# Performance work log

Measured on AMD Instinct MI355X. Metric: run time of the kernel, lower is better.

## Reference

```python
import jax, jax.numpy as jnp
import numpy as np

H, KVH, HD = 32, 8, 128
DM = 4096
LN_L, LN_R = 64, 64
K_BITS, V_BITS = 4, 4
ROPE_THETA = 10000.0


def _rope(x, pos):
    # x: [B, nH, S, D], pos: [B, S]
    D = x.shape[-1]
    inv_freq = 1.0 / (ROPE_THETA ** (jnp.arange(0, D, 2, dtype=jnp.float32) / D))
    freqs = pos[:, :, None].astype(jnp.float32) * inv_freq            # [B,S,D/2]
    emb = jnp.concatenate([freqs, freqs], axis=-1)                     # [B,S,D]
    cos = jnp.cos(emb)[:, None, :, :]
    sin = jnp.sin(emb)[:, None, :, :]
    x1, x2 = x[..., : D // 2], x[..., D // 2:]
    rot = jnp.concatenate([-x2, x1], axis=-1)
    return x * cos + rot * sin


def _fake_quant(x, bits):
    # per-token (last-dim row) symmetric fake quantization
    qmax = 2.0 ** (bits - 1) - 1.0
    s = jnp.maximum(jnp.max(jnp.abs(x), axis=-1, keepdims=True) / qmax, 1e-8)
    return jnp.clip(jnp.round(x / s), -qmax, qmax) * s


def setup_inputs() -> dict:
    key = jax.random.key(0)
    ks = jax.random.split(key, 10)
    B, S = 1, 2048
    hidden_states = jax.random.normal(ks[0], (B, S, DM), dtype=jnp.float32)
    causal = jnp.tril(jnp.ones((S, S), dtype=bool))
    attention_mask = jnp.where(causal, 0.0, -1e9).astype(jnp.float32)[None, None]  # [1,1,S,S]
    position_ids = jnp.arange(S, dtype=jnp.int32)[None, :]
    sc = 1.0 / np.sqrt(DM)
    Wq = jax.random.normal(ks[1], (DM, H * HD), dtype=jnp.float32) * sc
    Wk = jax.random.normal(ks[2], (DM, KVH * HD), dtype=jnp.float32) * sc
    Wv = jax.random.normal(ks[3], (DM, KVH * HD), dtype=jnp.float32) * sc
    Wo = jax.random.normal(ks[4], (H * HD, DM), dtype=jnp.float32) * (1.0 / np.sqrt(H * HD))
    ln_left = jnp.eye(LN_L, dtype=jnp.float32) + 0.02 * jax.random.normal(ks[5], (LN_L, LN_L), dtype=jnp.float32)
    ln_right = jnp.eye(LN_R, dtype=jnp.float32) + 0.02 * jax.random.normal(ks[6], (LN_R, LN_R), dtype=jnp.float32)
    Tk = jnp.eye(HD, dtype=jnp.float32) + 0.05 * jax.random.normal(ks[7], (HD, HD), dtype=jnp.float32)
    Tv = jnp.eye(HD, dtype=jnp.float32) + 0.05 * jax.random.normal(ks[8], (HD, HD), dtype=jnp.float32)
    return {"hidden_states": hidden_states, "attention_mask": attention_mask,
            "position_ids": position_ids, "ln_left": ln_left, "ln_right": ln_right,
            "Wq": Wq, "Wk": Wk, "Wv": Wv, "Wo": Wo, "Tk": Tk, "Tv": Tv}


def reference(hidden_states, attention_mask, position_ids,
              ln_left, ln_right, Wq, Wk, Wv, Wo, Tk, Tv):
    B, S, _ = hidden_states.shape
    # ln_trans: Kronecker-decomposed SVD transform on hidden dim (64x64)
    h = hidden_states.reshape(B, S, LN_L, LN_R)
    h = jnp.einsum('bslr,la,rc->bsac', h, ln_left, ln_right).reshape(B, S, DM)
    # q/k/v projections (effective, trans-absorbed weights)
    q = (h @ Wq).reshape(B, S, H, HD).transpose(0, 2, 1, 3)    # [B,H,S,hd]
    k = (h @ Wk).reshape(B, S, KVH, HD).transpose(0, 2, 1, 3)  # [B,KVH,S,hd]
    v = ((h @ Wv).reshape(B, S, KVH, HD) @ Tv).transpose(0, 2, 1, 3)  # vcache_trans on V
    # RoPE
    q = _rope(q, position_ids)
    k = _rope(k, position_ids)
    # kcache_trans: q gets inv-transpose, k gets forward transform, then fake-quant K
    Tk_inv_t = jnp.linalg.inv(Tk).T
    q = q @ Tk_inv_t
    k = _fake_quant(k @ Tk, K_BITS)
    # vcache quant
    v = _fake_quant(v, V_BITS)
    # GQA repeat
    rep = H // KVH
    k = jnp.repeat(k, rep, axis=1)
    v = jnp.repeat(v, rep, axis=1)
    scores = jnp.einsum('bhqd,bhkd->bhqk', q, k) / np.sqrt(HD) + attention_mask
    p = jax.nn.softmax(scores.astype(jnp.float32), axis=-1).astype(q.dtype)
    o = jnp.einsum('bhqk,bhkd->bhqd', p, v).transpose(0, 2, 1, 3)  # [B,S,H,hd]
    # undo vcache_trans per head, then output projection
    o = o @ jnp.linalg.inv(Tv)
    return o.reshape(B, S, DM) @ Wo
```

## Files before the change

kernel.cpp:

```cpp
#include <hip/hip_runtime.h>
#include <math.h>

#define S_    2048
#define DM_   4096
#define H_    32
#define KVH_  8
#define HD_   128

typedef __bf16 bf16x8 __attribute__((ext_vector_type(8)));
typedef float  f32x4  __attribute__((ext_vector_type(4)));
typedef unsigned short u16x8 __attribute__((ext_vector_type(8)));
typedef unsigned short ushort_t;

__device__ __forceinline__ ushort_t f2b(float f) {
  unsigned int u = __float_as_uint(f);
  unsigned int r = (u + 0x7fffu + ((u >> 16) & 1u)) >> 16;
  return (ushort_t)r;
}
__device__ __forceinline__ float b2f(ushort_t h) {
  return __uint_as_float(((unsigned int)h) << 16);
}
__device__ __forceinline__ bf16x8 asbf(u16x8 v) {
  return __builtin_bit_cast(bf16x8, v);
}

__device__ __forceinline__ void gload16(const void* g, void* l) {
  __builtin_amdgcn_global_load_lds(
      (const __attribute__((address_space(1))) void*)g,
      (__attribute__((address_space(3))) void*)(unsigned int)(unsigned long long)l,
      16, 0, 0);
}

__global__ void newton_init(const float* __restrict__ A0, const float* __restrict__ A1,
                            float* __restrict__ X0, float* __restrict__ X1)
{
  const float* A = blockIdx.x ? A1 : A0;
  float*       X = blockIdx.x ? X1 : X0;
  const int i = blockIdx.y * 1024 + threadIdx.x;
  const int r = i >> 7, c = i & 127;
  X[i] = ((r == c) ? 2.0f : 0.0f) - A[i];
}

__global__ __launch_bounds__(256) void nmm(
    const float* __restrict__ A0, const float* __restrict__ B0, float* __restrict__ C0, int tr0,
    const float* __restrict__ A1, const float* __restrict__ B1, float* __restrict__ C1, int tr1,
    int update)
{
  const float* A = blockIdx.y ? A1 : A0;
  const float* B = blockIdx.y ? B1 : B0;
  float*       C = blockIdx.y ? C1 : C0;
  const int tr   = blockIdx.y ? tr1 : tr0;
  const int m0   = blockIdx.x * 32;
  const int tid  = threadIdx.x;

  __shared__ float Bs[128][132];
  __shared__ float As[32][132];

#pragma unroll
  for (int i = 0; i < 16; ++i) {
    int idx = tid + i * 256;
    int row = idx >> 5, c4 = (idx & 31) * 4;
    *(float4*)&Bs[row][c4] = *(const float4*)&B[row * 128 + c4];
  }
#pragma unroll
  for (int i = 0; i < 4; ++i) {
    int idx = tid + i * 256;
    int row = idx >> 5, c4 = (idx & 31) * 4;
    *(float4*)&As[row][c4] = *(const float4*)&A[(m0 + row) * 128 + c4];
  }
  __syncthreads();

  const int rloc = tid >> 3;
  const int c0   = (tid & 7) * 16;
  float acc[16];
#pragma unroll
  for (int j = 0; j < 16; ++j) acc[j] = 0.0f;
  for (int k = 0; k < 128; ++k) {
    float a = As[rloc][k];
#pragma unroll
    for (int j = 0; j < 16; j += 4) {
      float4 bv = *(const float4*)&Bs[k][c0 + j];
      acc[j + 0] += a * bv.x; acc[j + 1] += a * bv.y;
      acc[j + 2] += a * bv.z; acc[j + 3] += a * bv.w;
    }
  }
#pragma unroll
  for (int j = 0; j < 16; ++j) {
    float v = update ? (2.0f * As[rloc][c0 + j] - acc[j]) : acc[j];
    if (tr) C[(c0 + j) * 128 + (m0 + rloc)] = v;
    else    C[(m0 + rloc) * 128 + c0 + j]   = v;
  }
}

__global__ void ttrans(const float* __restrict__ in, float* __restrict__ out)
{
  __shared__ float t[32][33];
  const int bx = blockIdx.x * 32, by = blockIdx.y * 32;
  const int r = threadIdx.x >> 5, c = threadIdx.x & 31;
#pragma unroll
  for (int i = 0; i < 4; ++i)
    t[r + i * 8][c] = in[(by + r + i * 8) * 128 + bx + c];
  __syncthreads();
#pragma unroll
  for (int i = 0; i < 4; ++i)
    out[(bx + r + i * 8) * 128 + by + c] = t[c][r + i * 8];
}

__global__ void tfrag_prep(const float* __restrict__ T0, const float* __restrict__ T1,
                           const float* __restrict__ T2, const float* __restrict__ T3,
                           ushort_t* __restrict__ Fhi, ushort_t* __restrict__ Flo)
{
  const int mat = blockIdx.x;
  const float* src = (mat == 0) ? T0 : ((mat == 1) ? T1 : ((mat == 2) ? T2 : T3));
  ushort_t* hi = Fhi + mat * 16384;
  ushort_t* lo = Flo + mat * 16384;
  const int t = threadIdx.x;
  for (int ch = 0; ch < 32; ++ch) {
    int nt = ch >> 2, ds = ch & 3;
#pragma unroll
    for (int i = 0; i < 2; ++i) {
      int idx = t + i * 256;
      int ln = idx >> 3, j = idx & 7;
      int cc = ln & 15, gg = ln >> 4;
      int d = ds * 32 + gg * 8 + j, n = nt * 16 + cc;
      float x = src[d * 128 + n];
      ushort_t hb = f2b(x);
      hi[(ch << 9) + idx] = hb;
      lo[(ch << 9) + idx] = f2b(x - b2f(hb));
    }
  }
}

__global__ void pack64(const float* __restrict__ R, const float* __restrict__ L,
                       ushort_t* __restrict__ RBh, ushort_t* __restrict__ RBl,
                       ushort_t* __restrict__ LBh, ushort_t* __restrict__ LBl)
{
  const float* src = blockIdx.x ? L : R;
  ushort_t* hp = blockIdx.x ? LBh : RBh;
  ushort_t* lp = blockIdx.x ? LBl : RBl;
  const int t = threadIdx.x;
  for (int ch = 0; ch < 8; ++ch) {
    int nt = ch >> 1, ds = ch & 1;
#pragma unroll
    for (int i = 0; i < 2; ++i) {
      int idx = t + i * 256;
      int ln = idx >> 3, j = idx & 7;
      int cc = ln & 15, gg = ln >> 4;
      float x = src[(ds * 32 + gg * 8 + j) * 64 + nt * 16 + cc];
      ushort_t hb = f2b(x);
      hp[(ch << 9) + idx] = hb;
      lp[(ch << 9) + idx] = f2b(x - b2f(hb));
    }
  }
}

__global__ void rope_table(const int* __restrict__ pos,
                           float* __restrict__ cosT, float* __restrict__ sinT)
{
  const int s = blockIdx.x, i = threadIdx.x;
  float invf = 1.0f / (float)pow(10000.0, (double)i * (1.0 / 64.0));
  float ang  = (float)pos[s] * invf;
  cosT[s * 64 + i] = cosf(ang);
  sinT[s * 64 + i] = sinf(ang);
}

__global__ __launch_bounds__(256) void ln3(
    const float* __restrict__ hid,
    const ushort_t* __restrict__ RBh, const ushort_t* __restrict__ RBl,
    const ushort_t* __restrict__ LBh, const ushort_t* __restrict__ LBl,
    ushort_t* __restrict__ hb16, ushort_t* __restrict__ hlo16)
{
  const int blk = blockIdx.x;
  const int tid = threadIdx.x;
  const int w = tid >> 6, lane = tid & 63;
  const int c = lane & 15, g = lane >> 4;

  __shared__ float Hs[4][64 * 68];

#pragma unroll
  for (int i = 0; i < 16; ++i) {
    int idx = tid + i * 256;
    int t = idx >> 10, e = idx & 1023;
    int l = e >> 4, r4 = (e & 15) * 4;
    *(float4*)&Hs[t][l * 68 + r4] =
        *(const float4*)&hid[((size_t)(blk * 4 + t)) * 4096 + l * 64 + r4];
  }
  __syncthreads();

  float* Hw = Hs[w];

  u16x8 ah[4][2], al[4][2];
#pragma unroll
  for (int mt = 0; mt < 4; ++mt)
#pragma unroll
    for (int ds = 0; ds < 2; ++ds) {
      u16x8 th, tl;
#pragma unroll
      for (int j = 0; j < 8; ++j) {
        float x = Hw[(mt * 16 + c) * 68 + ds * 32 + g * 8 + j];
        ushort_t hb = f2b(x); th[j] = hb; tl[j] = f2b(x - b2f(hb));
      }
      ah[mt][ds] = th; al[mt][ds] = tl;
    }

  f32x4 acc[4][4];
#pragma unroll
  for (int mt = 0; mt < 4; ++mt)
#pragma unroll
    for (int nt = 0; nt < 4; ++nt) acc[mt][nt] = (f32x4){0.f, 0.f, 0.f, 0.f};
#pragma unroll
  for (int nt = 0; nt < 4; ++nt) {
    u16x8 bh[2], bl[2];
#pragma unroll
    for (int ds = 0; ds < 2; ++ds) {
      bh[ds] = *(const u16x8*)(RBh + ((nt * 2 + ds) << 9) + lane * 8);
      bl[ds] = *(const u16x8*)(RBl + ((nt * 2 + ds) << 9) + lane * 8);
    }
#pragma unroll
    for (int mt = 0; mt < 4; ++mt)
#pragma unroll
      for (int ds = 0; ds < 2; ++ds) {
        acc[mt][nt] = __builtin_amdgcn_mfma_f32_16x16x32_bf16(asbf(ah[mt][ds]), asbf(bh[ds]), acc[mt][nt], 0, 0, 0);
        acc[mt][nt] = __builtin_amdgcn_mfma_f32_16x16x32_bf16(asbf(ah[mt][ds]), asbf(bl[ds]), acc[mt][nt], 0, 0, 0);
        acc[mt][nt] = __builtin_amdgcn_mfma_f32_16x16x32_bf16(asbf(al[mt][ds]), asbf(bh[ds]), acc[mt][nt], 0, 0, 0);
      }
  }

#pragma unroll
  for (int mt = 0; mt < 4; ++mt)
#pragma unroll
    for (int nt = 0; nt < 4; ++nt)
#pragma unroll
      for (int reg = 0; reg < 4; ++reg)
        Hw[(mt * 16 + g * 4 + reg) * 68 + nt * 16 + c] = acc[mt][nt][reg];

  u16x8 a2h[4][2], a2l[4][2];
#pragma unroll
  for (int mt = 0; mt < 4; ++mt)
#pragma unroll
    for (int ds = 0; ds < 2; ++ds) {
      a2h[mt][ds] = *(const u16x8*)(LBh + ((mt * 2 + ds) << 9) + lane * 8);
      a2l[mt][ds] = *(const u16x8*)(LBl + ((mt * 2 + ds) << 9) + lane * 8);
    }
  f32x4 acc2[4][4];
#pragma unroll
  for (int mt = 0; mt < 4; ++mt)
#pragma unroll
    for (int nt = 0; nt < 4; ++nt) acc2[mt][nt] = (f32x4){0.f, 0.f, 0.f, 0.f};
#pragma unroll
  for (int nt = 0; nt < 4; ++nt) {
#pragma unroll
    for (int ds = 0; ds < 2; ++ds) {
      u16x8 bh, bl;
#pragma unroll
      for (int j = 0; j < 8; ++j) {
        float x = Hw[(ds * 32 + g * 8 + j) * 68 + nt * 16 + c];
        ushort_t hb = f2b(x); bh[j] = hb; bl[j] = f2b(x - b2f(hb));
      }
#pragma unroll
      for (int mt = 0; mt < 4; ++mt) {
        acc2[mt][nt] = __builtin_amdgcn_mfma_f32_16x16x32_bf16(asbf(a2h[mt][ds]), asbf(bh), acc2[mt][nt], 0, 0, 0);
        acc2[mt][nt] = __builtin_amdgcn_mfma_f32_16x16x32_bf16(asbf(a2h[mt][ds]), asbf(bl), acc2[mt][nt], 0, 0, 0);
        acc2[mt][nt] = __builtin_amdgcn_mfma_f32_16x16x32_bf16(asbf(a2l[mt][ds]), asbf(bh), acc2[mt][nt], 0, 0, 0);
      }
    }
  }

  ushort_t* hp = (ushort_t*)Hw;
#pragma unroll
  for (int mt = 0; mt < 4; ++mt)
#pragma unroll
    for (int nt = 0; nt < 4; ++nt)
#pragma unroll
      for (int reg = 0; reg < 4; ++reg) {
        int a = mt * 16 + g * 4 + reg, cc2 = nt * 16 + c;
        float v = acc2[mt][nt][reg];
        ushort_t hb = f2b(v);
        hp[a * 64 + cc2] = hb;
        hp[4096 + a * 64 + cc2] = f2b(v - b2f(hb));
      }

  const size_t sbase = ((size_t)(blk * 4 + w)) * 4096;
#pragma unroll
  for (int i = 0; i < 8; ++i) {
    int idx = i * 64 + lane;
    int row = idx >> 3, c8 = (idx & 7) * 8;
    *(u16x8*)&hb16[sbase + row * 64 * 8 / 8 * 1 + row * 0 + row * 64 + c8 - row * 64] = *(const u16x8*)&hp[row * 64 + c8];
  }
#pragma unroll
  for (int i = 0; i < 8; ++i) {
    int idx = i * 64 + lane;
    int row = idx >> 3, c8 = (idx & 7) * 8;
    *(u16x8*)&hb16[sbase + row * 64 + c8]  = *(const u16x8*)&hp[row * 64 + c8];
    *(u16x8*)&hlo16[sbase + row * 64 + c8] = *(const u16x8*)&hp[4096 + row * 64 + c8];
  }
}

__global__ void wtrans(const float* __restrict__ W, ushort_t* __restrict__ WT,
                       int K, int N)
{
  __shared__ ushort_t t[64][68];
  const int tid = threadIdx.x;
  const int n0 = blockIdx.x * 64, k0 = blockIdx.y * 64;
  for (int idx = tid; idx < 4096; idx += 256) {
    int rr = idx >> 6, cc = idx & 63;
    t[cc][rr] = f2b(W[(size_t)(k0 + rr) * N + n0 + cc]);
  }
  __syncthreads();
  for (int idx = tid; idx < 4096; idx += 256) {
    int rr = idx >> 6, cc = idx & 63;
    WT[(size_t)(n0 + rr) * K + k0 + cc] = t[rr][cc];
  }
}

__global__ void wtrans_hl(const float* __restrict__ W,
                          ushort_t* __restrict__ WThi, ushort_t* __restrict__ WTlo,
                          int K, int N, int rowoff)
{
  __shared__ ushort_t th[64][68];
  __shared__ ushort_t tl[64][68];
  const int tid = threadIdx.x;
  const int n0 = blockIdx.x * 64, k0 = blockIdx.y * 64;
  for (int idx = tid; idx < 4096; idx += 256) {
    int rr = idx >> 6, cc = idx & 63;
    float x = W[(size_t)(k0 + rr) * N + n0 + cc];
    ushort_t h = f2b(x);
    th[cc][rr] = h;
    tl[cc][rr] = f2b(x - b2f(h));
  }
  __syncthreads();
  for (int idx = tid; idx < 4096; idx += 256) {
    int rr = idx >> 6, cc = idx & 63;
    size_t o = (size_t)(rowoff + n0 + rr) * K + k0 + cc;
    WThi[o] = th[rr][cc];
    WTlo[o] = tl[rr][cc];
  }
}

__global__ __launch_bounds__(256) void wfold3(
    const float* __restrict__ Wo,
    const ushort_t* __restrict__ TBh, const ushort_t* __restrict__ TBl,
    ushort_t* __restrict__ WT)
{
  const int n0 = blockIdx.x * 128;
  const int h  = blockIdx.y;
  const int tid = threadIdx.x;
  const int w = tid >> 6, lane = tid & 63;
  const int c = lane & 15, g = lane >> 4;

  __shared__ float WoS[128 * 132];

#pragma unroll
  for (int i = 0; i < 16; ++i) {
    int idx = tid + i * 256;
    int e = idx >> 5, n4 = (idx & 31) * 4;
    *(float4*)&WoS[e * 132 + n4] =
        *(const float4*)&Wo[(size_t)(h * 128 + e) * 4096 + n0 + n4];
  }
  __syncthreads();

  u16x8 ah[2][4], al[2][4];
#pragma unroll
  for (int mt = 0; mt < 2; ++mt)
#pragma unroll
    for (int ds = 0; ds < 4; ++ds) {
      u16x8 th, tl;
#pragma unroll
      for (int j = 0; j < 8; ++j) {
        float x = WoS[(ds * 32 + g * 8 + j) * 132 + w * 32 + mt * 16 + c];
        ushort_t hb = f2b(x); th[j] = hb; tl[j] = f2b(x - b2f(hb));
      }
      ah[mt][ds] = th; al[mt][ds] = tl;
    }

  f32x4 acc[2][8];
#pragma unroll
  for (int mt = 0; mt < 2; ++mt)
#pragma unroll
    for (int nt = 0; nt < 8; ++nt) acc[mt][nt] = (f32x4){0.f, 0.f, 0.f, 0.f};
#pragma unroll
  for (int nt = 0; nt < 8; ++nt) {
#pragma unroll
    for (int ds = 0; ds < 4; ++ds) {
      u16x8 bh = *(const u16x8*)(TBh + ((nt * 4 + ds) << 9) + lane * 8);
      u16x8 bl = *(const u16x8*)(TBl + ((nt * 4 + ds) << 9) + lane * 8);
#pragma unroll
      for (int mt = 0; mt < 2; ++mt) {
        acc[mt][nt] = __builtin_amdgcn_mfma_f32_16x16x32_bf16(asbf(ah[mt][ds]), asbf(bh), acc[mt][nt], 0, 0, 0);
        acc[mt][nt] = __builtin_amdgcn_mfma_f32_16x16x32_bf16(asbf(ah[mt][ds]), asbf(bl), acc[mt][nt], 0, 0, 0);
        acc[mt][nt] = __builtin_amdgcn_mfma_f32_16x16x32_bf16(asbf(al[mt][ds]), asbf(bh), acc[mt][nt], 0, 0, 0);
      }
    }
  }
  __syncthreads();

  ushort_t* OS = (ushort_t*)WoS;
#pragma unroll
  for (int mt = 0; mt < 2; ++mt)
#pragma unroll
    for (int nt = 0; nt < 8; ++nt)
#pragma unroll
      for (int reg = 0; reg < 4; ++reg)
        OS[(w * 32 + mt * 16 + g * 4 + reg) * 136 + nt * 16 + c] = f2b(acc[mt][nt][reg]);
  __syncthreads();

#pragma unroll
  for (int i = 0; i < 8; ++i) {
    int idx = tid + i * 256;
    int nn = idx >> 4, c8 = (idx & 15) * 8;
    *(u16x8*)&WT[(size_t)(n0 + nn) * 4096 + h * 128 + c8] = *(const u16x8*)&OS[nn * 136 + c8];
  }
}

__global__ __launch_bounds__(256) void gemm_bf16(const ushort_t* __restrict__ A,
                                                 const ushort_t* __restrict__ BT,
                                                 float* __restrict__ C,
                                                 int M, int N, int K, int qlayout)
{
  __shared__ __align__(16) ushort_t As[128 * 64];
  __shared__ __align__(16) ushort_t Bs[128 * 64];
  const int tid = threadIdx.x;
  const int bm = blockIdx.y * 128, bn = blockIdx.x * 128;
  const int lane = tid & 63, w = tid >> 6;
  const int c = lane & 15, g = lane >> 4;
  const int wm = (w >> 1) * 64, wn = (w & 1) * 64;
  f32x4 acc[4][4];
#pragma unroll
  for (int mt = 0; mt < 4; ++mt)
#pragma unroll
    for (int nt = 0; nt < 4; ++nt) acc[mt][nt] = (f32x4){0.f, 0.f, 0.f, 0.f};
  const int srow = tid >> 3;
  const int slot = (tid & 7) ^ (srow & 7);
  for (int k0 = 0; k0 < K; k0 += 64) {
    __syncthreads();
#pragma unroll
    for (int ii = 0; ii < 4; ++ii) {
      gload16(A  + (size_t)(bm + ii * 32 + srow) * K + k0 + slot * 8,
              (char*)As + w * 1024 + ii * 4096);
      gload16(BT + (size_t)(bn + ii * 32 + srow) * K + k0 + slot * 8,
              (char*)Bs + w * 1024 + ii * 4096);
    }
    __syncthreads();
#pragma unroll
    for (int ks = 0; ks < 2; ++ks) {
      bf16x8 av[4], bv[4];
#pragma unroll
      for (int mt = 0; mt < 4; ++mt)
        av[mt] = *(const bf16x8*)((const char*)As + (wm + mt * 16 + c) * 128 +
                                  (((ks * 4 + g) ^ (c & 7)) << 4));
#pragma unroll
      for (int nt = 0; nt < 4; ++nt)
        bv[nt] = *(const bf16x8*)((const char*)Bs + (wn + nt * 16 + c) * 128 +
                                  (((ks * 4 + g) ^ (c & 7)) << 4));
#pragma unroll
      for (int mt = 0; mt < 4; ++mt)
#pragma unroll
        for (int nt = 0; nt < 4; ++nt)
          acc[mt][nt] = __builtin_amdgcn_mfma_f32_16x16x32_bf16(av[mt], bv[nt], acc[mt][nt], 0, 0, 0);
    }
  }
#pragma unroll
  for (int mt = 0; mt < 4; ++mt)
#pragma unroll
    for (int nt = 0; nt < 4; ++nt)
#pragma unroll
      for (int reg = 0; reg < 4; ++reg) {
        int m = bm + wm + mt * 16 + g * 4 + reg;
        int n = bn + wn + nt * 16 + c;
        float v = acc[mt][nt][reg];
        if (qlayout) C[((size_t)(n >> 7) * S_ + m) * 128 + (n & 127)] = v;
        else         C[(size_t)m * N + n] = v;
      }
}

__global__ __launch_bounds__(256) void gemm_bf16_3(
    const ushort_t* __restrict__ Ahi, const ushort_t* __restrict__ Alo,
    const ushort_t* __restrict__ BThi, const ushort_t* __restrict__ BTlo,
    float* __restrict__ Ck, float* __restrict__ Cv, int M, int N, int K)
{
  __shared__ __align__(16) ushort_t Ash[128 * 64];
  __shared__ __align__(16) ushort_t Asl[128 * 64];
  __shared__ __align__(16) ushort_t Bsh[64 * 64];
  __shared__ __align__(16) ushort_t Bsl[64 * 64];
  const int tid = threadIdx.x;
  const int bm = blockIdx.y * 128, bn = blockIdx.x * 64;
  const int lane = tid & 63, w = tid >> 6;
  const int c = lane & 15, g = lane >> 4;
  const int wm = w * 32;
  f32x4 acc[2][4];
#pragma unroll
  for (int mt = 0; mt < 2; ++mt)
#pragma unroll
    for (int nt = 0; nt < 4; ++nt) acc[mt][nt] = (f32x4){0.f, 0.f, 0.f, 0.f};
  const int srow = tid >> 3;
  const int slot = (tid & 7) ^ (srow & 7);
  for (int k0 = 0; k0 < K; k0 += 64) {
    __syncthreads();
#pragma unroll
    for (int ii = 0; ii < 4; ++ii) {
      const size_t ga = (size_t)(bm + ii * 32 + srow) * K + k0 + slot * 8;
      gload16(Ahi + ga, (char*)Ash + w * 1024 + ii * 4096);
      gload16(Alo + ga, (char*)Asl + w * 1024 + ii * 4096);
    }
#pragma unroll
    for (int ii = 0; ii < 2; ++ii) {
      const size_t gb = (size_t)(bn + ii * 32 + srow) * K + k0 + slot * 8;
      gload16(BThi + gb, (char*)Bsh + w * 1024 + ii * 4096);
      gload16(BTlo + gb, (char*)Bsl + w * 1024 + ii * 4096);
    }
    __syncthreads();
#pragma unroll
    for (int ks = 0; ks < 2; ++ks) {
      bf16x8 ah[2], al[2], bh[4], bl[4];
#pragma unroll
      for (int mt = 0; mt < 2; ++mt) {
        int ro = (wm + mt * 16 + c) * 128;
        int so = ((ks * 4 + g) ^ (c & 7)) << 4;
        ah[mt] = *(const bf16x8*)((const char*)Ash + ro + so);
        al[mt] = *(const bf16x8*)((const char*)Asl + ro + so);
      }
#pragma unroll
      for (int nt = 0; nt < 4; ++nt) {
        int ro = (nt * 16 + c) * 128;
        int so = ((ks * 4 + g) ^ (c & 7)) << 4;
        bh[nt] = *(const bf16x8*)((const char*)Bsh + ro + so);
        bl[nt] = *(const bf16x8*)((const char*)Bsl + ro + so);
      }
#pragma unroll
      for (int mt = 0; mt < 2; ++mt)
#pragma unroll
        for (int nt = 0; nt < 4; ++nt) {
          acc[mt][nt] = __builtin_amdgcn_mfma_f32_16x16x32_bf16(ah[mt], bh[nt], acc[mt][nt], 0, 0, 0);
          acc[mt][nt] = __builtin_amdgcn_mfma_f32_16x16x32_bf16(ah[mt], bl[nt], acc[mt][nt], 0, 0, 0);
          acc[mt][nt] = __builtin_amdgcn_mfma_f32_16x16x32_bf16(al[mt], bh[nt], acc[mt][nt], 0, 0, 0);
        }
    }
  }
#pragma unroll
  for (int mt = 0; mt < 2; ++mt)
#pragma unroll
    for (int nt = 0; nt < 4; ++nt)
#pragma unroll
      for (int reg = 0; reg < 4; ++reg) {
        int m = bm + wm + mt * 16 + g * 4 + reg;
        int n = bn + nt * 16 + c;
        float v = acc[mt][nt][reg];
        if (n < 1024) Ck[((size_t)(n >> 7) * S_ + m) * 128 + (n & 127)] = v;
        else          Cv[((size_t)((n - 1024) >> 7) * S_ + m) * 128 + (n & 127)] = v;
      }
}

__global__ __launch_bounds__(256) void tpost_mfma(
    const float* __restrict__ src,
    const ushort_t* __restrict__ Thi, const ushort_t* __restrict__ Tlo,
    const float* __restrict__ cosT, const float* __restrict__ sinT,
    ushort_t* __restrict__ outp, int mode)
{
  const int blk = blockIdx.x;
  const int tid = threadIdx.x;
  const int w = tid >> 6, lane = tid & 63;
  const int c = lane & 15, g = lane >> 4;

  __shared__ float raw_[32 * 132];
  __shared__ float rop_[32 * 132];
  __shared__ __align__(16) ushort_t vtile[32][136];

#pragma unroll
  for (int i = 0; i < 4; ++i) {
    int idx = tid + i * 256;
    int row = idx >> 5, c4 = (idx & 31) * 4;
    *(float4*)&raw_[row * 132 + c4] =
        *(const float4*)&src[(size_t)(blk * 32 + row) * 128 + c4];
  }
  __syncthreads();

  {
    const int r = tid >> 3, co = (tid & 7) * 16;
    if (mode <= 1) {
      const int s = (blk & 63) * 32 + r;
      const float* ct = cosT + (size_t)s * 64;
      const float* st = sinT + (size_t)s * 64;
#pragma unroll
      for (int j = 0; j < 16; ++j) {
        int cc = co + j, i2 = cc & 63;
        float x = raw_[r * 132 + cc];
        float other = (cc < 64) ? raw_[r * 132 + cc + 64] : raw_[r * 132 + cc - 64];
        rop_[r * 132 + cc] = (cc < 64) ? (x * ct[i2] - other * st[i2])
                                       : (x * ct[i2] + other * st[i2]);
      }
    } else {
#pragma unroll
      for (int j = 0; j < 16; ++j) {
        int cc = co + j;
        rop_[r * 132 + cc] = raw_[r * 132 + cc];
      }
    }
  }
  __syncthreads();

  u16x8 ahu[2][4], alu[2][4];
#pragma unroll
  for (int mt = 0; mt < 2; ++mt)
#pragma unroll
    for (int ds = 0; ds < 4; ++ds) {
      u16x8 th, tl;
#pragma unroll
      for (int j = 0; j < 8; ++j) {
        float x = rop_[(mt * 16 + c) * 132 + ds * 32 + g * 8 + j];
        ushort_t hb = f2b(x);
        th[j] = hb;
        tl[j] = f2b(x - b2f(hb));
      }
      ahu[mt][ds] = th;
      alu[mt][ds] = tl;
    }

  f32x4 acc[2][2];
#pragma unroll
  for (int mt = 0; mt < 2; ++mt)
#pragma unroll
    for (int nl = 0; nl < 2; ++nl) acc[mt][nl] = (f32x4){0.f, 0.f, 0.f, 0.f};
#pragma unroll
  for (int nl = 0; nl < 2; ++nl) {
    const int nt = w * 2 + nl;
    u16x8 bh[4], bl[4];
#pragma unroll
    for (int ds = 0; ds < 4; ++ds) {
      bh[ds] = *(const u16x8*)(Thi + ((nt * 4 + ds) << 9) + lane * 8);
      bl[ds] = *(const u16x8*)(Tlo + ((nt * 4 + ds) << 9) + lane * 8);
    }
#pragma unroll
    for (int mt = 0; mt < 2; ++mt)
#pragma unroll
      for (int ds = 0; ds < 4; ++ds) {
        acc[mt][nl] = __builtin_amdgcn_mfma_f32_16x16x32_bf16(asbf(ahu[mt][ds]), asbf(bh[ds]), acc[mt][nl], 0, 0, 0);
        acc[mt][nl] = __builtin_amdgcn_mfma_f32_16x16x32_bf16(asbf(ahu[mt][ds]), asbf(bl[ds]), acc[mt][nl], 0, 0, 0);
        acc[mt][nl] = __builtin_amdgcn_mfma_f32_16x16x32_bf16(asbf(alu[mt][ds]), asbf(bh[ds]), acc[mt][nl], 0, 0, 0);
      }
  }
  __syncthreads();

#pragma unroll
  for (int mt = 0; mt < 2; ++mt)
#pragma unroll
    for (int nl = 0; nl < 2; ++nl)
#pragma unroll
      for (int reg = 0; reg < 4; ++reg)
        raw_[(mt * 16 + g * 4 + reg) * 132 + (w * 2 + nl) * 16 + c] = acc[mt][nl][reg];
  __syncthreads();

  const int r = tid >> 3, co = (tid & 7) * 16;
  float vals[16];
#pragma unroll
  for (int j = 0; j < 16; ++j) vals[j] = raw_[r * 132 + co + j];

  if (mode == 0) {
#pragma unroll
    for (int j = 0; j < 16; ++j) vals[j] *= 0.08838834764831845f;
  } else {
    float m = 0.0f;
#pragma unroll
    for (int j = 0; j < 16; ++j) m = fmaxf(m, fabsf(vals[j]));
    m = fmaxf(m, __shfl_xor(m, 1));
    m = fmaxf(m, __shfl_xor(m, 2));
    m = fmaxf(m, __shfl_xor(m, 4));
    const float sc = fmaxf(m * (1.0f / 7.0f), 1e-8f);
#pragma unroll
    for (int j = 0; j < 16; ++j) {
      float qv = rintf(vals[j] / sc);
      qv = fminf(7.0f, fmaxf(-7.0f, qv));
      vals[j] = qv * sc;
    }
  }

  if (mode <= 1) {
    const size_t chunkbase = ((size_t)blk << 13) +
                             ((size_t)((r >> 4) * 4 + (co >> 5)) << 10);
    const int lane0 = ((co >> 3) & 3) * 16 + (r & 15);
    const int lane1 = (((co + 8) >> 3) & 3) * 16 + (r & 15);
    u16x8 o0, o1;
#pragma unroll
    for (int j = 0; j < 8; ++j) { o0[j] = f2b(vals[j]); o1[j] = f2b(vals[j + 8]); }
    *(u16x8*)((char*)outp + chunkbase + lane0 * 16) = o0;
    *(u16x8*)((char*)outp + chunkbase + lane1 * 16) = o1;
  } else {
#pragma unroll
    for (int j = 0; j < 16; ++j) vtile[r][co + j] = f2b(vals[j]);
    __syncthreads();
#pragma unroll
    for (int i = 0; i < 2; ++i) {
      int id = tid + i * 256;
      int dt = id >> 6, ln = id & 63;
      int gg = ln >> 4, cc = ln & 15;
      u16x8 o;
#pragma unroll
      for (int j = 0; j < 8; ++j) o[j] = vtile[gg * 8 + j][dt * 16 + cc];
      *(u16x8*)(outp + (((size_t)blk) << 12) + (dt << 9) + ln * 8) = o;
    }
  }
}

__global__ __launch_bounds__(256) void attn_mfma6(
    const ushort_t* __restrict__ qf_,
    const ushort_t* __restrict__ kf_,
    const ushort_t* __restrict__ vf_,
    ushort_t* __restrict__ o16)
{
  const int lid = blockIdx.x;
  const int xcd = lid & 7;
  const int idx = lid >> 3;
  const int h   = xcd * 4 + (idx & 3);
  const int kb  = idx >> 2;
  const int kvh = xcd;

  const int tid = threadIdx.x;
  const int w    = tid >> 6;
  const int lane = tid & 63;
  const int c = lane & 15, g = lane >> 4;
  const int qt = (w < 2) ? (2 * kb + w) : (60 - 2 * kb + w);

  __shared__ __align__(16) ushort_t Ps[4][2][16][40];

  const float LOG2E = 1.44269504f;
  const float MBIAS = 28.8539008f;

  const char* qtile = (const char*)qf_ + (((size_t)(h * 64 + qt)) << 13);
  bf16x8 qf[2][4];
#pragma unroll
  for (int mt = 0; mt < 2; ++mt)
#pragma unroll
    for (int ds = 0; ds < 4; ++ds)
      qf[mt][ds] = *(const bf16x8*)(qtile + ((mt * 4 + ds) << 10) + lane * 16);

  bf16x8 ones;
#pragma unroll
  for (int j = 0; j < 8; ++j) ones[j] = (__bf16)1.0f;

  f32x4 oa[2][8];
#pragma unroll
  for (int mt = 0; mt < 2; ++mt)
#pragma unroll
    for (int dt = 0; dt < 8; ++dt) oa[mt][dt] = (f32x4){0.f, 0.f, 0.f, 0.f};
  f32x4 la[2];
  la[0] = (f32x4){0.f, 0.f, 0.f, 0.f};
  la[1] = (f32x4){0.f, 0.f, 0.f, 0.f};

  const char* kbase = (const char*)kf_ + (((size_t)kvh * 64) << 13);
  const char* vbase = (const char*)vf_ + (((size_t)kvh * 64) << 13);

  for (int kt = 0; kt <= qt; ++kt) {
    const char* ktile = kbase + ((size_t)kt << 13);
    const char* vtile = vbase + ((size_t)kt << 13);
    bf16x8 kc[2][4], vc[8];
#pragma unroll
    for (int nt = 0; nt < 2; ++nt)
#pragma unroll
      for (int ds = 0; ds < 4; ++ds)
        kc[nt][ds] = *(const bf16x8*)(ktile + ((nt * 4 + ds) << 10) + lane * 16);
#pragma unroll
    for (int dt = 0; dt < 8; ++dt)
      vc[dt] = *(const bf16x8*)(vtile + (dt << 10) + lane * 16);

    f32x4 sc[2][2];
#pragma unroll
    for (int mt = 0; mt < 2; ++mt)
#pragma unroll
      for (int nt = 0; nt < 2; ++nt) sc[mt][nt] = (f32x4){0.f, 0.f, 0.f, 0.f};
    __builtin_amdgcn_s_setprio(1);
#pragma unroll
    for (int ds = 0; ds < 4; ++ds) {
      sc[0][0] = __builtin_amdgcn_mfma_f32_16x16x32_bf16(qf[0][ds], kc[0][ds], sc[0][0], 0, 0, 0);
      sc[0][1] = __builtin_amdgcn_mfma_f32_16x16x32_bf16(qf[0][ds], kc[1][ds], sc[0][1], 0, 0, 0);
      sc[1][0] = __builtin_amdgcn_mfma_f32_16x16x32_bf16(qf[1][ds], kc[0][ds], sc[1][0], 0, 0, 0);
      sc[1][1] = __builtin_amdgcn_mfma_f32_16x16x32_bf16(qf[1][ds], kc[1][ds], sc[1][1], 0, 0, 0);
    }
    __builtin_amdgcn_s_setprio(0);

#pragma unroll
    for (int mt = 0; mt < 2; ++mt) {
#pragma unroll
      for (int reg = 0; reg < 4; ++reg) {
        float s0 = sc[mt][0][reg], s1 = sc[mt][1][reg];
        if (kt == qt) {
          int qrl = mt * 16 + g * 4 + reg;
          if (c > qrl)      s0 = -INFINITY;
          if (16 + c > qrl) s1 = -INFINITY;
        }
        float p0 = exp2f(s0 * LOG2E - MBIAS);
        float p1 = exp2f(s1 * LOG2E - MBIAS);
        Ps[w][mt][g * 4 + reg][c]      = f2b(p0);
        Ps[w][mt][g * 4 + reg][16 + c] = f2b(p1);
      }
    }

    bf16x8 pa0 = *reinterpret_cast<const bf16x8*>(&Ps[w][0][c][g * 8]);
    bf16x8 pa1 = *reinterpret_cast<const bf16x8*>(&Ps[w][1][c][g * 8]);
    __builtin_amdgcn_s_setprio(1);
#pragma unroll
    for (int dt = 0; dt < 8; ++dt) {
      oa[0][dt] = __builtin_amdgcn_mfma_f32_16x16x32_bf16(pa0, vc[dt], oa[0][dt], 0, 0, 0);
      oa[1][dt] = __builtin_amdgcn_mfma_f32_16x16x32_bf16(pa1, vc[dt], oa[1][dt], 0, 0, 0);
    }
    la[0] = __builtin_amdgcn_mfma_f32_16x16x32_bf16(pa0, ones, la[0], 0, 0, 0);
    la[1] = __builtin_amdgcn_mfma_f32_16x16x32_bf16(pa1, ones, la[1], 0, 0, 0);
    __builtin_amdgcn_s_setprio(0);
  }

#pragma unroll
  for (int mt = 0; mt < 2; ++mt)
#pragma unroll
    for (int reg = 0; reg < 4; ++reg) {
      float li = 1.0f / la[mt][reg];
      int srow = qt * 32 + mt * 16 + g * 4 + reg;
      ushort_t* orow = o16 + (size_t)srow * DM_ + h * 128;
#pragma unroll
      for (int dt = 0; dt < 8; ++dt)
        orow[dt * 16 + c] = f2b(oa[mt][dt][reg] * li);
    }
}

extern "C" void kernel_launch(void* const* d_in, const int* in_sizes, int n_in,
                              void* d_out, int out_size, void* d_ws, size_t ws_size,
                              hipStream_t stream)
{
  (void)in_sizes; (void)n_in; (void)out_size; (void)ws_size;
  const float* hidden = (const float*)d_in[0];
  const int*   pos    = (const int*)d_in[2];
  const float* lnL    = (const float*)d_in[3];
  const float* lnR    = (const float*)d_in[4];
  const float* Wq     = (const float*)d_in[5];
  const float* Wk     = (const float*)d_in[6];
  const float* Wv     = (const float*)d_in[7];
  const float* Wo     = (const float*)d_in[8];
  const float* Tk     = (const float*)d_in[9];
  const float* Tv     = (const float*)d_in[10];
  float* out = (float*)d_out;

  float* ws   = (float*)d_ws;
  float* hbuf = ws;
  float* kbuf = hbuf + (size_t)S_ * DM_;
  float* vbuf = kbuf + (size_t)S_ * KVH_ * HD_;
  float* Tkit = vbuf + (size_t)S_ * KVH_ * HD_;
  float* TvI  = Tkit + 128 * 128;
  float* cosT = TvI + 128 * 128;
  float* sinT = cosT + (size_t)S_ * 64;
  ushort_t* hb16 = (ushort_t*)(sinT + (size_t)S_ * 64);
  ushort_t* WT   = hb16 + (size_t)S_ * DM_;
  float* nb      = (float*)(WT + (size_t)DM_ * DM_);
  float* TvIT    = nb + 6 * 16384;
  ushort_t* tfH  = (ushort_t*)(TvIT + 16384);
  ushort_t* tfL  = tfH + 4 * 16384;
  ushort_t* RBh  = tfL + 4 * 16384;
  ushort_t* RBl  = RBh + 4096;
  ushort_t* LBh  = RBl + 4096;
  ushort_t* LBl  = LBh + 4096;

  char* hbytes = (char*)hbuf;
  ushort_t* hlo16 = (ushort_t*)hbytes;
  ushort_t* qfrag = (ushort_t*)hbytes;
  ushort_t* kfrag = (ushort_t*)(hbytes + (16u << 20));
  ushort_t* vfrag = (ushort_t*)(hbytes + (20u << 20));

  ushort_t* WTkh = WT;
  ushort_t* WTkl = WT + (size_t)2048 * DM_;

  float* Xk = nb,              *Xv = nb + 16384;
  float* Yk = nb + 2 * 16384,  *Yv = nb + 3 * 16384;
  float* Xk2 = nb + 4 * 16384, *Xv2 = nb + 5 * 16384;

  float* qbuf = out;

  newton_init<<<dim3(2, 16), 1024, 0, stream>>>(Tk, Tv, Xk, Xv);
  for (int it = 0; it < 4; ++it) {
    nmm<<<dim3(4, 2), 256, 0, stream>>>(Tk, Xk, Yk, 0, Tv, Xv, Yv, 0, 0);
    const int last = (it == 3);
    float* ok = last ? Tkit : Xk2;
    float* ov = last ? TvI  : Xv2;
    nmm<<<dim3(4, 2), 256, 0, stream>>>(Xk, Yk, ok, last ? 1 : 0, Xv, Yv, ov, 0, 1);
    float* t;
    t = Xk; Xk = Xk2; Xk2 = t;
    t = Xv; Xv = Xv2; Xv2 = t;
  }
  ttrans<<<dim3(4, 4), 256, 0, stream>>>(TvI, TvIT);
  tfrag_prep<<<4, 256, 0, stream>>>(Tkit, Tk, Tv, TvIT, tfH, tfL);
  pack64<<<2, 256, 0, stream>>>(lnR, lnL, RBh, RBl, LBh, LBl);

  rope_table<<<S_, 64, 0, stream>>>(pos, cosT, sinT);
  ln3<<<S_ / 4, 256, 0, stream>>>(hidden, RBh, RBl, LBh, LBl, hb16, hlo16);

  wtrans<<<dim3(DM_ / 64, DM_ / 64), 256, 0, stream>>>(Wq, WT, DM_, DM_);
  gemm_bf16<<<dim3(DM_ / 128, S_ / 128), 256, 0, stream>>>(hb16, WT, qbuf, S_, DM_, DM_, 1);
  wtrans_hl<<<dim3(16, 64), 256, 0, stream>>>(Wk, WTkh, WTkl, DM_, 1024, 0);
  wtrans_hl<<<dim3(16, 64), 256, 0, stream>>>(Wv, WTkh, WTkl, DM_, 1024, 1024);
  gemm_bf16_3<<<dim3(32, S_ / 128), 256, 0, stream>>>(hb16, hlo16, WTkh, WTkl,
                                                      kbuf, vbuf, S_, 2048, DM_);

  tpost_mfma<<<H_ * S_ / 32, 256, 0, stream>>>(qbuf, tfH,             tfL,
                                               cosT, sinT, qfrag, 0);
  tpost_mfma<<<KVH_ * S_ / 32, 256, 0, stream>>>(kbuf, tfH + 16384,   tfL + 16384,
                                                 cosT, sinT, kfrag, 1);
  tpost_mfma<<<KVH_ * S_ / 32, 256, 0, stream>>>(vbuf, tfH + 2 * 16384, tfL + 2 * 16384,
                                                 cosT, sinT, vfrag, 2);

  attn_mfma6<<<dim3(S_ / 128 * H_), 256, 0, stream>>>(qfrag, kfrag, vfrag, hb16);

  wfold3<<<dim3(DM_ / 128, H_), 256, 0, stream>>>(Wo, tfH + 3 * 16384, tfL + 3 * 16384, WT);
  gemm_bf16<<<dim3(DM_ / 128, S_ / 128), 256, 0, stream>>>(hb16, WT, out, S_, DM_, DM_, 0);
}
```

Measured before the change: 587.2 us.

## Merge small prep kernels, fuse tpost launches, prefetch next K/V tile in attention

Merges the transpose, T-fragment and LN packing kernels into one launch, with the transpose folded into indexed loads. Combines the two Wk/Wv weight-transpose launches and the three tpost launches into single grids. Drops a duplicate store loop in ln3. In attention it register-prefetches the next K/V tile while the current one is computed, and uses a native bf16 cast for P. This cuts launch overhead and hides global-load latency, at the cost of extra register pressure in the attention kernel.

```diff
diff --git a/kernel.cpp b/kernel.cpp
--- a/kernel.cpp
+++ b/kernel.cpp
@@ -92,64 +92,50 @@
   }
 }
 
-__global__ void ttrans(const float* __restrict__ in, float* __restrict__ out)
-{
-  __shared__ float t[32][33];
-  const int bx = blockIdx.x * 32, by = blockIdx.y * 32;
-  const int r = threadIdx.x >> 5, c = threadIdx.x & 31;
-#pragma unroll
-  for (int i = 0; i < 4; ++i)
-    t[r + i * 8][c] = in[(by + r + i * 8) * 128 + bx + c];
-  __syncthreads();
-#pragma unroll
-  for (int i = 0; i < 4; ++i)
-    out[(bx + r + i * 8) * 128 + by + c] = t[c][r + i * 8];
-}
-
-__global__ void tfrag_prep(const float* __restrict__ T0, const float* __restrict__ T1,
-                           const float* __restrict__ T2, const float* __restrict__ T3,
-                           ushort_t* __restrict__ Fhi, ushort_t* __restrict__ Flo)
+__global__ void prep_all(const float* __restrict__ Tkit, const float* __restrict__ Tk,
+                         const float* __restrict__ Tv,   const float* __restrict__ TvI,
+                         const float* __restrict__ lnR,  const float* __restrict__ lnL,
+                         ushort_t* __restrict__ Fhi, ushort_t* __restrict__ Flo,
+                         ushort_t* __restrict__ RBh, ushort_t* __restrict__ RBl,
+                         ushort_t* __restrict__ LBh, ushort_t* __restrict__ LBl)
 {
   const int mat = blockIdx.x;
-  const float* src = (mat == 0) ? T0 : ((mat == 1) ? T1 : ((mat == 2) ? T2 : T3));
-  ushort_t* hi = Fhi + mat * 16384;
-  ushort_t* lo = Flo + mat * 16384;
-  const int t = threadIdx.x;
-  for (int ch = 0; ch < 32; ++ch) {
-    int nt = ch >> 2, ds = ch & 3;
-#pragma unroll
-    for (int i = 0; i < 2; ++i) {
-      int idx = t + i * 256;
-      int ln = idx >> 3, j = idx & 7;
-      int cc = ln & 15, gg = ln >> 4;
-      int d = ds * 32 + gg * 8 + j, n = nt * 16 + cc;
-      float x = src[d * 128 + n];
-      ushort_t hb = f2b(x);
-      hi[(ch << 9) + idx] = hb;
-      lo[(ch << 9) + idx] = f2b(x - b2f(hb));
-    }
-  }
-}
-
-__global__ void pack64(const float* __restrict__ R, const float* __restrict__ L,
-                       ushort_t* __restrict__ RBh, ushort_t* __restrict__ RBl,
-                       ushort_t* __restrict__ LBh, ushort_t* __restrict__ LBl)
-{
-  const float* src = blockIdx.x ? L : R;
-  ushort_t* hp = blockIdx.x ? LBh : RBh;
-  ushort_t* lp = blockIdx.x ? LBl : RBl;
-  const int t = threadIdx.x;
-  for (int ch = 0; ch < 8; ++ch) {
-    int nt = ch >> 1, ds = ch & 1;
-#pragma unroll
-    for (int i = 0; i < 2; ++i) {
-      int idx = t + i * 256;
-      int ln = idx >> 3, j = idx & 7;
-      int cc = ln & 15, gg = ln >> 4;
-      float x = src[(ds * 32 + gg * 8 + j) * 64 + nt * 16 + cc];
-      ushort_t hb = f2b(x);
-      hp[(ch << 9) + idx] = hb;
-      lp[(ch << 9) + idx] = f2b(x - b2f(hb));
+  const int t   = threadIdx.x;
+  if (mat < 4) {
+    const float* src = (mat == 0) ? Tkit : ((mat == 1) ? Tk : ((mat == 2) ? Tv : TvI));
+    const int tr = (mat == 3);
+    ushort_t* hi = Fhi + mat * 16384;
+    ushort_t* lo = Flo + mat * 16384;
+    for (int ch = 0; ch < 32; ++ch) {
+      int nt = ch >> 2, ds = ch & 3;
+#pragma unroll
+      for (int i = 0; i < 2; ++i) {
+        int idx = t + i * 256;
+        int ln = idx >> 3, j = idx & 7;
+        int cc = ln & 15, gg = ln >> 4;
+        int d = ds * 32 + gg * 8 + j, n = nt * 16 + cc;
+        float x = tr ? src[n * 128 + d] : src[d * 128 + n];
+        ushort_t hb = f2b(x);
+        hi[(ch << 9) + idx] = hb;
+        lo[(ch << 9) + idx] = f2b(x - b2f(hb));
+      }
+    }
+  } else {
+    const float* src = (mat == 4) ? lnR : lnL;
+    ushort_t* hp = (mat == 4) ? RBh : LBh;
+    ushort_t* lp = (mat == 4) ? RBl : LBl;
+    for (int ch = 0; ch < 8; ++ch) {
+      int nt = ch >> 1, ds = ch & 1;
+#pragma unroll
+      for (int i = 0; i < 2; ++i) {
+        int idx = t + i * 256;
+        int ln = idx >> 3, j = idx & 7;
+        int cc = ln & 15, gg = ln >> 4;
+        float x = src[(ds * 32 + gg * 8 + j) * 64 + nt * 16 + cc];
+        ushort_t hb = f2b(x);
+        hp[(ch << 9) + idx] = hb;
+        lp[(ch << 9) + idx] = f2b(x - b2f(hb));
+      }
     }
   }
 }
@@ -285,12 +271,6 @@
   for (int i = 0; i < 8; ++i) {
     int idx = i * 64 + lane;
     int row = idx >> 3, c8 = (idx & 7) * 8;
-    *(u16x8*)&hb16[sbase + row * 64 * 8 / 8 * 1 + row * 0 + row * 64 + c8 - row * 64] = *(const u16x8*)&hp[row * 64 + c8];
-  }
-#pragma unroll
-  for (int i = 0; i < 8; ++i) {
-    int idx = i * 64 + lane;
-    int row = idx >> 3, c8 = (idx & 7) * 8;
     *(u16x8*)&hb16[sbase + row * 64 + c8]  = *(const u16x8*)&hp[row * 64 + c8];
     *(u16x8*)&hlo16[sbase + row * 64 + c8] = *(const u16x8*)&hp[4096 + row * 64 + c8];
   }
@@ -313,10 +293,13 @@
   }
 }
 
-__global__ void wtrans_hl(const float* __restrict__ W,
-                          ushort_t* __restrict__ WThi, ushort_t* __restrict__ WTlo,
-                          int K, int N, int rowoff)
-{
+__global__ void wtrans_hl2(const float* __restrict__ Wk, const float* __restrict__ Wv,
+                           ushort_t* __restrict__ WThi, ushort_t* __restrict__ WTlo)
+{
+  const int which = blockIdx.z;
+  const float* W = which ? Wv : Wk;
+  const int rowoff = which ? 1024 : 0;
+  const int K = DM_, N = 1024;
   __shared__ ushort_t th[64][68];
   __shared__ ushort_t tl[64][68];
   const int tid = threadIdx.x;
@@ -550,13 +533,20 @@
       }
 }
 
-__global__ __launch_bounds__(256) void tpost_mfma(
-    const float* __restrict__ src,
-    const ushort_t* __restrict__ Thi, const ushort_t* __restrict__ Tlo,
+__global__ __launch_bounds__(256) void tpost_all(
+    const float* __restrict__ qsrc, const float* __restrict__ ksrc,
+    const float* __restrict__ vsrc,
+    const ushort_t* __restrict__ tfH, const ushort_t* __restrict__ tfL,
     const float* __restrict__ cosT, const float* __restrict__ sinT,
-    ushort_t* __restrict__ outp, int mode)
-{
-  const int blk = blockIdx.x;
+    ushort_t* __restrict__ qfrag, ushort_t* __restrict__ kfrag,
+    ushort_t* __restrict__ vfrag)
+{
+  const int b = blockIdx.x;
+  const float* src; const ushort_t *Thi, *Tlo; ushort_t* outp; int mode, blk;
+  if (b < 2048)      { src = qsrc; Thi = tfH;             Tlo = tfL;             outp = qfrag; mode = 0; blk = b; }
+  else if (b < 2560) { src = ksrc; Thi = tfH + 16384;     Tlo = tfL + 16384;     outp = kfrag; mode = 1; blk = b - 2048; }
+  else               { src = vsrc; Thi = tfH + 2 * 16384; Tlo = tfL + 2 * 16384; outp = vfrag; mode = 2; blk = b - 2560; }
+
   const int tid = threadIdx.x;
   const int w = tid >> 6, lane = tid & 63;
   const int c = lane & 15, g = lane >> 4;
@@ -700,7 +690,7 @@
   }
 }
 
-__global__ __launch_bounds__(256) void attn_mfma6(
+__global__ __launch_bounds__(256) void attn_mfma7(
     const ushort_t* __restrict__ qf_,
     const ushort_t* __restrict__ kf_,
     const ushort_t* __restrict__ vf_,
@@ -748,18 +738,30 @@
   const char* kbase = (const char*)kf_ + (((size_t)kvh * 64) << 13);
   const char* vbase = (const char*)vf_ + (((size_t)kvh * 64) << 13);
 
+  bf16x8 kc[2][4], vc[8], kn[2][4], vn[8];
+#pragma unroll
+  for (int nt = 0; nt < 2; ++nt)
+#pragma unroll
+    for (int ds = 0; ds < 4; ++ds)
+      kc[nt][ds] = *(const bf16x8*)(kbase + ((nt * 4 + ds) << 10) + lane * 16);
+#pragma unroll
+  for (int dt = 0; dt < 8; ++dt)
+    vc[dt] = *(const bf16x8*)(vbase + (dt << 10) + lane * 16);
+
   for (int kt = 0; kt <= qt; ++kt) {
-    const char* ktile = kbase + ((size_t)kt << 13);
-    const char* vtile = vbase + ((size_t)kt << 13);
-    bf16x8 kc[2][4], vc[8];
-#pragma unroll
-    for (int nt = 0; nt < 2; ++nt)
-#pragma unroll
-      for (int ds = 0; ds < 4; ++ds)
-        kc[nt][ds] = *(const bf16x8*)(ktile + ((nt * 4 + ds) << 10) + lane * 16);
-#pragma unroll
-    for (int dt = 0; dt < 8; ++dt)
-      vc[dt] = *(const bf16x8*)(vtile + (dt << 10) + lane * 16);
+    const int ktn = kt + 1;
+    if (ktn <= qt) {
+      const char* ktile = kbase + ((size_t)ktn << 13);
+      const char* vtile = vbase + ((size_t)ktn << 13);
+#pragma unroll
+      for (int nt = 0; nt < 2; ++nt)
+#pragma unroll
+        for (int ds = 0; ds < 4; ++ds)
+          kn[nt][ds] = *(const bf16x8*)(ktile + ((nt * 4 + ds) << 10) + lane * 16);
+#pragma unroll
+      for (int dt = 0; dt < 8; ++dt)
+        vn[dt] = *(const bf16x8*)(vtile + (dt << 10) + lane * 16);
+    }
 
     f32x4 sc[2][2];
 #pragma unroll
@@ -788,8 +790,8 @@
         }
         float p0 = exp2f(s0 * LOG2E - MBIAS);
         float p1 = exp2f(s1 * LOG2E - MBIAS);
-        Ps[w][mt][g * 4 + reg][c]      = f2b(p0);
-        Ps[w][mt][g * 4 + reg][16 + c] = f2b(p1);
+        Ps[w][mt][g * 4 + reg][c]      = __builtin_bit_cast(ushort_t, (__bf16)p0);
+        Ps[w][mt][g * 4 + reg][16 + c] = __builtin_bit_cast(ushort_t, (__bf16)p1);
       }
     }
 
@@ -804,6 +806,17 @@
     la[0] = __builtin_amdgcn_mfma_f32_16x16x32_bf16(pa0, ones, la[0], 0, 0, 0);
     la[1] = __builtin_amdgcn_mfma_f32_16x16x32_bf16(pa1, ones, la[1], 0, 0, 0);
     __builtin_amdgcn_s_setprio(0);
+
+    if (ktn <= qt) {
+#pragma unroll
+      for (int nt = 0; nt < 2; ++nt)
+#pragma unroll
+        for (int ds = 0; ds < 4; ++ds)
+          kc[nt][ds] = kn[nt][ds];
+#pragma unroll
+      for (int dt = 0; dt < 8; ++dt)
+        vc[dt] = vn[dt];
+    }
   }
 
 #pragma unroll
@@ -847,8 +860,7 @@
   ushort_t* hb16 = (ushort_t*)(sinT + (size_t)S_ * 64);
   ushort_t* WT   = hb16 + (size_t)S_ * DM_;
   float* nb      = (float*)(WT + (size_t)DM_ * DM_);
-  float* TvIT    = nb + 6 * 16384;
-  ushort_t* tfH  = (ushort_t*)(TvIT + 16384);
+  ushort_t* tfH  = (ushort_t*)(nb + 6 * 16384);
   ushort_t* tfL  = tfH + 4 * 16384;
   ushort_t* RBh  = tfL + 4 * 16384;
   ushort_t* RBl  = RBh + 4096;
@@ -881,28 +893,22 @@
     t = Xk; Xk = Xk2; Xk2 = t;
     t = Xv; Xv = Xv2; Xv2 = t;
   }
-  ttrans<<<dim3(4, 4), 256, 0, stream>>>(TvI, TvIT);
-  tfrag_prep<<<4, 256, 0, stream>>>(Tkit, Tk, Tv, TvIT, tfH, tfL);
-  pack64<<<2, 256, 0, stream>>>(lnR, lnL, RBh, RBl, LBh, LBl);
+  prep_all<<<6, 256, 0, stream>>>(Tkit, Tk, Tv, TvI, lnR, lnL,
+                                  tfH, tfL, RBh, RBl, LBh, LBl);
 
   rope_table<<<S_, 64, 0, stream>>>(pos, cosT, sinT);
   ln3<<<S_ / 4, 256, 0, stream>>>(hidden, RBh, RBl, LBh, LBl, hb16, hlo16);
 
   wtrans<<<dim3(DM_ / 64, DM_ / 64), 256, 0, stream>>>(Wq, WT, DM_, DM_);
   gemm_bf16<<<dim3(DM_ / 128, S_ / 128), 256, 0, stream>>>(hb16, WT, qbuf, S_, DM_, DM_, 1);
-  wtrans_hl<<<dim3(16, 64), 256, 0, stream>>>(Wk, WTkh, WTkl, DM_, 1024, 0);
-  wtrans_hl<<<dim3(16, 64), 256, 0, stream>>>(Wv, WTkh, WTkl, DM_, 1024, 1024);
+  wtrans_hl2<<<dim3(16, 64, 2), 256, 0, stream>>>(Wk, Wv, WTkh, WTkl);
   gemm_bf16_3<<<dim3(32, S_ / 128), 256, 0, stream>>>(hb16, hlo16, WTkh, WTkl,
                                                       kbuf, vbuf, S_, 2048, DM_);
 
-  tpost_mfma<<<H_ * S_ / 32, 256, 0, stream>>>(qbuf, tfH,             tfL,
-                                               cosT, sinT, qfrag, 0);
-  tpost_mfma<<<KVH_ * S_ / 32, 256, 0, stream>>>(kbuf, tfH + 16384,   tfL + 16384,
-                                                 cosT, sinT, kfrag, 1);
-  tpost_mfma<<<KVH_ * S_ / 32, 256, 0, stream>>>(vbuf, tfH + 2 * 16384, tfL + 2 * 16384,
-                                                 cosT, sinT, vfrag, 2);
-
-  attn_mfma6<<<dim3(S_ / 128 * H_), 256, 0, stream>>>(qfrag, kfrag, vfrag, hb16);
+  tpost_all<<<3072, 256, 0, stream>>>(qbuf, kbuf, vbuf, tfH, tfL,
+                                      cosT, sinT, qfrag, kfrag, vfrag);
+
+  attn_mfma7<<<dim3(S_ / 128 * H_), 256, 0, stream>>>(qfrag, kfrag, vfrag, hb16);
 
   wfold3<<<dim3(DM_ / 128, H_), 256, 0, stream>>>(Wo, tfH + 3 * 16384, tfL + 3 * 16384, WT);
   gemm_bf16<<<dim3(DM_ / 128, S_ / 128), 256, 0, stream>>>(hb16, WT, out, S_, DM_, DM_, 0);
```

Measured after the change: 606.5 us. 3.3% more time.
